# Kernel tuning notes

Measured on AMD Instinct MI355X. Metric: run time of the kernel, lower is better.

The kernel has to match this reference:

```python
import jax, jax.numpy as jnp
import numpy as np

# MalConv-style dims: byte vocab, tiny embed, wide stride-=kernel gated conv
B, T, V, E, C, K, S, N = 8, 1048576, 257, 8, 128, 512, 512, 64


def setup_inputs() -> dict:
    key = jax.random.key(0)
    k1, k2, k3, k4 = jax.random.split(key, 4)
    x = jax.random.randint(k1, (B, T), 0, V, dtype=jnp.int32)
    emb = jax.random.normal(k2, (V, E), dtype=jnp.float32) * 0.02
    fan = 1.0 / np.sqrt(E * K)
    w1 = jax.random.normal(k3, (C, E, K), dtype=jnp.float32) * fan
    w2 = jax.random.normal(k4, (C, E, K), dtype=jnp.float32) * fan
    b1 = jnp.zeros((C,), jnp.float32)
    b2 = jnp.zeros((C,), jnp.float32)
    return {"x": x, "emb": emb, "w1": w1, "b1": b1, "w2": w2, "b2": b2}


def reference(x, emb, w1, b1, w2, b2):
    # preprocess: byte embedding -> (B, E, T)
    z = emb[x].transpose(0, 2, 1)
    dn = ("NCH", "OIH", "NCH")
    # GatedConvolution: c1 * sigmoid(c2), valid conv, stride S -> (B, C, L)
    c1 = jax.lax.conv_general_dilated(z, w1, (S,), "VALID", dimension_numbers=dn) + b1[None, :, None]
    c2 = jax.lax.conv_general_dilated(z, w2, (S,), "VALID", dimension_numbers=dn) + b2[None, :, None]
    g = c1 * jax.nn.sigmoid(c2)  # (B, C, L)
    L = g.shape[-1]
    # input-space position of each conv output window; patch assignment
    pos = jnp.arange(L, dtype=jnp.int32) * S
    patch_size = -(-T // N)  # ceil(T / num_patches)
    seg = jnp.clip(pos // patch_size, 0, N - 1)  # (L,)
    # per-patch max-over-time, per channel: segment_max over the L axis
    gl = g.transpose(2, 0, 1).reshape(L, B * C)  # (L, B*C)
    mv = jax.ops.segment_max(gl, seg, num_segments=N)  # (N, B*C)
    max_vals = mv.reshape(N, B, C).transpose(1, 0, 2)  # (B, N, C)
    return max_vals
```

## Files before the change

### kernel.cpp

```cpp
#include <hip/hip_runtime.h>
#include <hip/hip_bf16.h>
#include <math.h>


typedef __bf16 bf16x8 __attribute__((ext_vector_type(8)));
typedef float  f32x4  __attribute__((ext_vector_type(4)));

#define WS_WP_OFF   0
#define WS_EMB_OFF  (2u << 20)
#define WS_C_OFF    (4u << 20)

__device__ __forceinline__ void load_lds16(const void* g, void* l) {
    __builtin_amdgcn_global_load_lds(
        (const __attribute__((address_space(1))) void*)g,
        (__attribute__((address_space(3))) void*)l,
        16, 0, 0);
}

__global__ void prep_kernel(const float* __restrict__ w1,
                            const float* __restrict__ w2,
                            const float* __restrict__ emb,
                            uint4* __restrict__ Wp4,
                            __bf16* __restrict__ embp) {
    int bid = blockIdx.x;
    int tid = threadIdx.x;
    if (bid < 128) {
        __shared__ __bf16 lds[8192];
        int cb = bid & 7;
        int sB = bid >> 3;
        int c0 = cb << 5;
        const float* wsrc = (c0 < 128) ? (w1 + ((size_t)c0 << 12))
                                       : (w2 + ((size_t)(c0 - 128) << 12));
        int j4  = tid & 7;
        int pr0 = tid >> 3;
#pragma unroll
        for (int p = 0; p < 8; ++p) {
            int pair = p * 32 + pr0;
            int cl = pair >> 3, e = pair & 7;
            const float4 v = *(const float4*)(wsrc + (cl << 12) + (e << 9) + (sB << 5) + (j4 << 2));
            float vv[4] = {v.x, v.y, v.z, v.w};
#pragma unroll
            for (int jj = 0; jj < 4; ++jj) {
                int j = (j4 << 2) + jj;
                int qq = j >> 3, tt = j & 7;
                lds[(((qq << 3) + tt) * 32 + cl) * 8 + e] = (__bf16)vv[jj];
            }
        }
        __syncthreads();
        const uint4* l4 = (const uint4*)lds;
        int nhalf = cb & 1, nt = cb >> 1;
        int base = (nt << 15) + (sB << 11) + (nhalf << 5);
#pragma unroll
        for (int it = 0; it < 4; ++it) {
            int idx = it * 256 + tid;
            int qq = idx >> 8, tt = (idx >> 5) & 7, w = idx & 31;
            Wp4[base + (tt << 8) + (qq << 6) + w] = l4[idx];
        }
    } else {
        for (int i = tid; i < 2056; i += 256) embp[i] = (__bf16)emb[i];
    }
}

__global__ __launch_bounds__(256, 2)
void gemm_kernel(const int* __restrict__ x,
                 const __bf16* __restrict__ Wp,
                 const uint4* __restrict__ embp,
                 float* __restrict__ Cbuf,
                 int ksplit) {
    __shared__ uint4 ldsB[2][2048];
    __shared__ uint4 embl[257];

    const int tid  = threadIdx.x;
    const int wave = tid >> 6;
    const int lane = tid & 63;
    const int q    = lane >> 4;
    const int nl   = lane & 15;

    for (int i = tid; i < 257; i += 256) embl[i] = embp[i];

    const int bid = blockIdx.x;
    int mt, nt, kh, nsteps, s0;
    if (ksplit == 2) {
        mt = ((bid >> 6) << 3) | (bid & 7);
        int combo = (bid >> 3) & 7;
        kh = combo & 1; nt = combo >> 1;
        nsteps = 8; s0 = kh << 3;
    } else {
        mt = ((bid >> 5) << 3) | (bid & 7);
        nt = (bid >> 3) & 3;
        kh = 0; nsteps = 16; s0 = 0;
    }
    const int m0 = mt << 8;
    const int rA = m0 + (wave << 6) + nl;
    const char* WpBase = (const char*)Wp + ((size_t)nt << 19);

    const int* xp[4];
#pragma unroll
    for (int rg = 0; rg < 4; ++rg)
        xp[rg] = x + (size_t)(rA + (rg << 4)) * 512 + (q << 3);

    int4 xc[4][2];
#pragma unroll
    for (int rg = 0; rg < 4; ++rg) {
        const int* p = xp[rg] + (s0 << 5);
        xc[rg][0] = *(const int4*)p;
        xc[rg][1] = *(const int4*)(p + 4);
    }
    {
        const char* src = WpBase + ((size_t)s0 << 15) + tid * 16;
        char* dst = (char*)&ldsB[0][0] + tid * 16;
#pragma unroll
        for (int i = 0; i < 8; ++i) load_lds16(src + i * 4096, dst + i * 4096);
    }
    __syncthreads();

    f32x4 acc[4][4] = {};

    for (int ss = 0; ss < nsteps; ++ss) {
        const int sp  = s0 + ss;
        const int buf = ss & 1;
        if (ss + 1 < nsteps) {
            const char* src = WpBase + ((size_t)(sp + 1) << 15) + tid * 16;
            char* dst = (char*)&ldsB[buf ^ 1][0] + tid * 16;
#pragma unroll
            for (int i = 0; i < 8; ++i) load_lds16(src + i * 4096, dst + i * 4096);
        }
        int idx[4][8];
#pragma unroll
        for (int rg = 0; rg < 4; ++rg) {
            idx[rg][0] = xc[rg][0].x; idx[rg][1] = xc[rg][0].y;
            idx[rg][2] = xc[rg][0].z; idx[rg][3] = xc[rg][0].w;
            idx[rg][4] = xc[rg][1].x; idx[rg][5] = xc[rg][1].y;
            idx[rg][6] = xc[rg][1].z; idx[rg][7] = xc[rg][1].w;
        }
        const int spn = (ss + 1 < nsteps) ? sp + 1 : sp;
#pragma unroll
        for (int rg = 0; rg < 4; ++rg) {
            const int* p = xp[rg] + (spn << 5);
            xc[rg][0] = *(const int4*)p;
            xc[rg][1] = *(const int4*)(p + 4);
        }
        const char* Bbase = (const char*)&ldsB[buf][0] + (q << 10) + (nl << 4);
#pragma unroll
        for (int t = 0; t < 8; ++t) {
            bf16x8 a[4];
#pragma unroll
            for (int rg = 0; rg < 4; ++rg)
                a[rg] = *reinterpret_cast<const bf16x8*>(&embl[idx[rg][t]]);
#pragma unroll
            for (int nf = 0; nf < 4; ++nf) {
                bf16x8 b = *reinterpret_cast<const bf16x8*>(Bbase + (t << 12) + (nf << 8));
#pragma unroll
                for (int rg = 0; rg < 4; ++rg)
                    acc[rg][nf] = __builtin_amdgcn_mfma_f32_16x16x32_bf16(a[rg], b, acc[rg][nf], 0, 0, 0);
            }
        }
        __syncthreads();
    }

    float* Cout = Cbuf + (size_t)kh * (16384 * 256);
#pragma unroll
    for (int rg = 0; rg < 4; ++rg) {
        int rowb = m0 + (wave << 6) + (rg << 4) + (q << 2);
#pragma unroll
        for (int nf = 0; nf < 4; ++nf) {
            int col = (nt << 6) + (nf << 4) + nl;
#pragma unroll
            for (int i = 0; i < 4; ++i)
                Cout[(size_t)(rowb + i) * 256 + col] = acc[rg][nf][i];
        }
    }
}

__global__ void reduce_kernel(const float* __restrict__ Cbuf,
                              const float* __restrict__ b1,
                              const float* __restrict__ b2,
                              float* __restrict__ out,
                              int ksplit) {
    __shared__ float sm[256];
    int tid = threadIdx.x;
    int c   = tid & 127;
    int lh  = tid >> 7;
    int gp  = blockIdx.x;
    float bb1 = b1[c], bb2 = b2[c];
    const float* base0 = Cbuf + (size_t)(gp * 32 + lh * 16) * 256 + c;
    const float* base1 = base0 + (size_t)16384 * 256;
    const bool ks2 = (ksplit == 2);
    float best = -INFINITY;
#pragma unroll 4
    for (int l = 0; l < 16; ++l) {
        float c1 = base0[0]   + bb1;
        float c2 = base0[128] + bb2;
        if (ks2) { c1 += base1[0]; c2 += base1[128]; }
        float g = c1 * (1.0f / (1.0f + __expf(-c2)));
        best = fmaxf(best, g);
        base0 += 256; base1 += 256;
    }
    sm[tid] = best;
    __syncthreads();
    if (lh == 0) out[(size_t)gp * 128 + c] = fmaxf(sm[tid], sm[tid + 128]);
}

extern "C" void kernel_launch(void* const* d_in, const int* in_sizes, int n_in,
                              void* d_out, int out_size, void* d_ws, size_t ws_size,
                              hipStream_t stream) {
    const int*   x   = (const int*)d_in[0];
    const float* emb = (const float*)d_in[1];
    const float* w1  = (const float*)d_in[2];
    const float* b1  = (const float*)d_in[3];
    const float* w2  = (const float*)d_in[4];
    const float* b2  = (const float*)d_in[5];
    float* out = (float*)d_out;

    char* ws = (char*)d_ws;
    __bf16* Wp   = (__bf16*)(ws + WS_WP_OFF);
    __bf16* embp = (__bf16*)(ws + WS_EMB_OFF);
    float*  Cbuf = (float*)(ws + WS_C_OFF);

    const size_t need2 = (size_t)(4u << 20) + 2ull * 16384 * 256 * 4;
    int ksplit = (ws_size >= need2) ? 2 : 1;

    prep_kernel<<<129, 256, 0, stream>>>(w1, w2, emb, (uint4*)Wp, embp);
    gemm_kernel<<<256 * ksplit, 256, 0, stream>>>(x, Wp, (const uint4*)embp, Cbuf, ksplit);
    reduce_kernel<<<512, 256, 0, stream>>>(Cbuf, b1, b2, out, ksplit);
}
```

Baseline: 124.2 us.

## Fuse gating and segment max into GEMM epilogue, drop split-K and reduce kernel

Weight packing now interleaves w1 and w2 channels so each N-tile holds matching c1/c2 columns. The GEMM epilogue applies the bias, the sigmoid gate and the per-patch max through cross-lane shuffles, and writes the final output directly. This removes the 32 MB intermediate C buffer and the separate reduce kernel. Split-K is dropped, so only 256 blocks run over 256 CUs with a full K loop each, at the risk of lower parallelism and longer per-block latency.

```diff
diff --git a/kernel.cpp b/kernel.cpp
--- a/kernel.cpp
+++ b/kernel.cpp
@@ -8,7 +8,6 @@
 
 #define WS_WP_OFF   0
 #define WS_EMB_OFF  (2u << 20)
-#define WS_C_OFF    (4u << 20)
 
 __device__ __forceinline__ void load_lds16(const void* g, void* l) {
     __builtin_amdgcn_global_load_lds(
@@ -28,16 +27,15 @@
         __shared__ __bf16 lds[8192];
         int cb = bid & 7;
         int sB = bid >> 3;
-        int c0 = cb << 5;
-        const float* wsrc = (c0 < 128) ? (w1 + ((size_t)c0 << 12))
-                                       : (w2 + ((size_t)(c0 - 128) << 12));
+        int nt = cb >> 1, nhalf = cb & 1;
+        const float* wsrc = (nhalf ? w2 : w1) + ((size_t)(nt << 5) << 12);
         int j4  = tid & 7;
         int pr0 = tid >> 3;
 #pragma unroll
         for (int p = 0; p < 8; ++p) {
             int pair = p * 32 + pr0;
             int cl = pair >> 3, e = pair & 7;
-            const float4 v = *(const float4*)(wsrc + (cl << 12) + (e << 9) + (sB << 5) + (j4 << 2));
+            const float4 v = *(const float4*)(wsrc + ((size_t)cl << 12) + (e << 9) + (sB << 5) + (j4 << 2));
             float vv[4] = {v.x, v.y, v.z, v.w};
 #pragma unroll
             for (int jj = 0; jj < 4; ++jj) {
@@ -48,7 +46,6 @@
         }
         __syncthreads();
         const uint4* l4 = (const uint4*)lds;
-        int nhalf = cb & 1, nt = cb >> 1;
         int base = (nt << 15) + (sB << 11) + (nhalf << 5);
 #pragma unroll
         for (int it = 0; it < 4; ++it) {
@@ -61,12 +58,13 @@
     }
 }
 
-__global__ __launch_bounds__(256, 2)
+__global__ __launch_bounds__(256, 1)
 void gemm_kernel(const int* __restrict__ x,
                  const __bf16* __restrict__ Wp,
                  const uint4* __restrict__ embp,
-                 float* __restrict__ Cbuf,
-                 int ksplit) {
+                 const float* __restrict__ b1,
+                 const float* __restrict__ b2,
+                 float* __restrict__ out) {
     __shared__ uint4 ldsB[2][2048];
     __shared__ uint4 embl[257];
 
@@ -79,17 +77,8 @@
     for (int i = tid; i < 257; i += 256) embl[i] = embp[i];
 
     const int bid = blockIdx.x;
-    int mt, nt, kh, nsteps, s0;
-    if (ksplit == 2) {
-        mt = ((bid >> 6) << 3) | (bid & 7);
-        int combo = (bid >> 3) & 7;
-        kh = combo & 1; nt = combo >> 1;
-        nsteps = 8; s0 = kh << 3;
-    } else {
-        mt = ((bid >> 5) << 3) | (bid & 7);
-        nt = (bid >> 3) & 3;
-        kh = 0; nsteps = 16; s0 = 0;
-    }
+    const int mt = ((bid >> 5) << 3) | (bid & 7);
+    const int nt = (bid >> 3) & 3;
     const int m0 = mt << 8;
     const int rA = m0 + (wave << 6) + nl;
     const char* WpBase = (const char*)Wp + ((size_t)nt << 19);
@@ -102,12 +91,11 @@
     int4 xc[4][2];
 #pragma unroll
     for (int rg = 0; rg < 4; ++rg) {
-        const int* p = xp[rg] + (s0 << 5);
-        xc[rg][0] = *(const int4*)p;
-        xc[rg][1] = *(const int4*)(p + 4);
+        xc[rg][0] = *(const int4*)xp[rg];
+        xc[rg][1] = *(const int4*)(xp[rg] + 4);
     }
     {
-        const char* src = WpBase + ((size_t)s0 << 15) + tid * 16;
+        const char* src = WpBase + tid * 16;
         char* dst = (char*)&ldsB[0][0] + tid * 16;
 #pragma unroll
         for (int i = 0; i < 8; ++i) load_lds16(src + i * 4096, dst + i * 4096);
@@ -116,10 +104,9 @@
 
     f32x4 acc[4][4] = {};
 
-    for (int ss = 0; ss < nsteps; ++ss) {
-        const int sp  = s0 + ss;
-        const int buf = ss & 1;
-        if (ss + 1 < nsteps) {
+    for (int sp = 0; sp < 16; ++sp) {
+        const int buf = sp & 1;
+        if (sp + 1 < 16) {
             const char* src = WpBase + ((size_t)(sp + 1) << 15) + tid * 16;
             char* dst = (char*)&ldsB[buf ^ 1][0] + tid * 16;
 #pragma unroll
@@ -133,7 +120,7 @@
             idx[rg][4] = xc[rg][1].x; idx[rg][5] = xc[rg][1].y;
             idx[rg][6] = xc[rg][1].z; idx[rg][7] = xc[rg][1].w;
         }
-        const int spn = (ss + 1 < nsteps) ? sp + 1 : sp;
+        const int spn = (sp + 1 < 16) ? sp + 1 : sp;
 #pragma unroll
         for (int rg = 0; rg < 4; ++rg) {
             const int* p = xp[rg] + (spn << 5);
@@ -158,47 +145,37 @@
         __syncthreads();
     }
 
-    float* Cout = Cbuf + (size_t)kh * (16384 * 256);
+    float bb1[2], bb2[2];
 #pragma unroll
-    for (int rg = 0; rg < 4; ++rg) {
-        int rowb = m0 + (wave << 6) + (rg << 4) + (q << 2);
+    for (int nf = 0; nf < 2; ++nf) {
+        int ch = (nt << 5) + (nf << 4) + nl;
+        bb1[nf] = b1[ch];
+        bb2[nf] = b2[ch];
+    }
 #pragma unroll
-        for (int nf = 0; nf < 4; ++nf) {
-            int col = (nt << 6) + (nf << 4) + nl;
+    for (int ph = 0; ph < 2; ++ph) {
 #pragma unroll
-            for (int i = 0; i < 4; ++i)
-                Cout[(size_t)(rowb + i) * 256 + col] = acc[rg][nf][i];
+        for (int nf = 0; nf < 2; ++nf) {
+            float v = -INFINITY;
+#pragma unroll
+            for (int rh = 0; rh < 2; ++rh) {
+                int rg = (ph << 1) + rh;
+#pragma unroll
+                for (int i = 0; i < 4; ++i) {
+                    float c1 = acc[rg][nf][i] + bb1[nf];
+                    float c2 = acc[rg][nf + 2][i] + bb2[nf];
+                    float g = c1 * (1.0f / (1.0f + __expf(-c2)));
+                    v = fmaxf(v, g);
+                }
+            }
+            v = fmaxf(v, __shfl_xor(v, 16));
+            v = fmaxf(v, __shfl_xor(v, 32));
+            if (lane < 16) {
+                int P = (mt << 3) + (wave << 1) + ph;
+                out[(size_t)P * 128 + (nt << 5) + (nf << 4) + nl] = v;
+            }
         }
     }
-}
-
-__global__ void reduce_kernel(const float* __restrict__ Cbuf,
-                              const float* __restrict__ b1,
-                              const float* __restrict__ b2,
-                              float* __restrict__ out,
-                              int ksplit) {
-    __shared__ float sm[256];
-    int tid = threadIdx.x;
-    int c   = tid & 127;
-    int lh  = tid >> 7;
-    int gp  = blockIdx.x;
-    float bb1 = b1[c], bb2 = b2[c];
-    const float* base0 = Cbuf + (size_t)(gp * 32 + lh * 16) * 256 + c;
-    const float* base1 = base0 + (size_t)16384 * 256;
-    const bool ks2 = (ksplit == 2);
-    float best = -INFINITY;
-#pragma unroll 4
-    for (int l = 0; l < 16; ++l) {
-        float c1 = base0[0]   + bb1;
-        float c2 = base0[128] + bb2;
-        if (ks2) { c1 += base1[0]; c2 += base1[128]; }
-        float g = c1 * (1.0f / (1.0f + __expf(-c2)));
-        best = fmaxf(best, g);
-        base0 += 256; base1 += 256;
-    }
-    sm[tid] = best;
-    __syncthreads();
-    if (lh == 0) out[(size_t)gp * 128 + c] = fmaxf(sm[tid], sm[tid + 128]);
 }
 
 extern "C" void kernel_launch(void* const* d_in, const int* in_sizes, int n_in,
@@ -215,12 +192,7 @@
     char* ws = (char*)d_ws;
     __bf16* Wp   = (__bf16*)(ws + WS_WP_OFF);
     __bf16* embp = (__bf16*)(ws + WS_EMB_OFF);
-    float*  Cbuf = (float*)(ws + WS_C_OFF);
-
-    const size_t need2 = (size_t)(4u << 20) + 2ull * 16384 * 256 * 4;
-    int ksplit = (ws_size >= need2) ? 2 : 1;
 
     prep_kernel<<<129, 256, 0, stream>>>(w1, w2, emb, (uint4*)Wp, embp);
-    gemm_kernel<<<256 * ksplit, 256, 0, stream>>>(x, Wp, (const uint4*)embp, Cbuf, ksplit);
-    reduce_kernel<<<512, 256, 0, stream>>>(Cbuf, b1, b2, out, ksplit);
+    gemm_kernel<<<256, 256, 0, stream>>>(x, Wp, (const uint4*)embp, b1, b2, out);
 }
```

After: 125.8 us. About the same (+1.3%).
